# Kernel tuning notes

Measured on AMD Instinct MI355X. Metric: run time of the kernel, lower is better.

The kernel has to match this reference:

```python
import jax, jax.numpy as jnp
import numpy as np

B, S, D, F, E, K, H = 4, 1024, 512, 2048, 8, 2, 8
HEAD_DIM = D // H


def setup_inputs() -> dict:
    key = jax.random.key(0)
    ks = jax.random.split(key, 8)
    s = 0.02
    return {
        "x": jax.random.normal(ks[0], (B, S, D), jnp.float32),
        "gate_Wk": jax.random.normal(ks[1], (D, D), jnp.float32) * s,
        "gate_bk": jnp.zeros((D,), jnp.float32),
        "expert_queries": jax.random.normal(ks[2], (E, D), jnp.float32),
        "Wqkv": jax.random.normal(ks[3], (E, 3 * D, D), jnp.float32) * s,
        "bqkv": jnp.zeros((E, 3 * D), jnp.float32),
        "Wo": jax.random.normal(ks[4], (E, D, D), jnp.float32) * s,
        "bo": jnp.zeros((E, D), jnp.float32),
        "g1": jnp.ones((E, D), jnp.float32),
        "be1": jnp.zeros((E, D), jnp.float32),
        "W1": jax.random.normal(ks[5], (E, F, D), jnp.float32) * s,
        "bf1": jnp.zeros((E, F), jnp.float32),
        "W2": jax.random.normal(ks[6], (E, D, F), jnp.float32) * s,
        "bf2": jnp.zeros((E, D), jnp.float32),
        "g2": jnp.ones((E, D), jnp.float32),
        "be2": jnp.zeros((E, D), jnp.float32),
    }


def _layernorm(x, g, b):
    m = x.mean(-1, keepdims=True)
    v = ((x - m) ** 2).mean(-1, keepdims=True)
    return (x - m) * jax.lax.rsqrt(v + 1e-5) * g + b


def _expert(x, Wqkv, bqkv, Wo, bo, g1, be1, W1, bf1, W2, bf2, g2, be2):
    # x: [B,S,D]; one ExpertTransformerDecoder block (dropout=0, eval)
    b, s, d = x.shape
    qkv = x @ Wqkv.T + bqkv                      # [B,S,3D]
    q, k, v = jnp.split(qkv, 3, axis=-1)
    to_heads = lambda t: t.reshape(b, s, H, HEAD_DIM).transpose(0, 2, 1, 3)
    q, k, v = to_heads(q), to_heads(k), to_heads(v)
    scale = 1.0 / np.sqrt(HEAD_DIM).astype(np.float32)
    attn = jax.nn.softmax(jnp.einsum('bhqd,bhkd->bhqk', q * scale, k), axis=-1)
    ctx = jnp.einsum('bhqk,bhkd->bhqd', attn, v).transpose(0, 2, 1, 3).reshape(b, s, d)
    ctx = ctx @ Wo.T + bo
    x = _layernorm(x + ctx, g1, be1)
    h = jax.nn.gelu(x @ W1.T + bf1, approximate=False)
    h = jax.nn.gelu(h @ W2.T + bf2, approximate=False)
    return _layernorm(x + h, g2, be2)


def reference(x, gate_Wk, gate_bk, expert_queries, Wqkv, bqkv, Wo, bo,
              g1, be1, W1, bf1, W2, bf2, g2, be2):
    # attention gating: softmax over experts of <key_proj(x), expert_q> * d^-0.5
    keys = x @ gate_Wk.T + gate_bk                      # [B,S,D]
    scores = jnp.einsum('bsd,ed->bse', keys, expert_queries) * (D ** -0.5)
    probs = jax.nn.softmax(scores, axis=-1)             # [B,S,E]
    # top-k mask + renormalize
    _, idx = jax.lax.top_k(probs, K)                    # [B,S,K]
    mask = jax.nn.one_hot(idx, E, dtype=probs.dtype).sum(-2)
    gated = probs * mask
    gated = gated / (gated.sum(-1, keepdims=True) + 1e-9)
    # run all experts densely (as the torch code does), vmapped over E
    eo = jax.vmap(_expert, in_axes=(None,) + (0,) * 12)(
        x, Wqkv, bqkv, Wo, bo, g1, be1, W1, bf1, W2, bf2, g2, be2)  # [E,B,S,D]
    return jnp.einsum('ebsd,bse->bsd', eo, gated)
```

## Files before the change

kernel.cpp:

```cpp
#include <hip/hip_runtime.h>
#include <cstdint>
#include <cmath>

#define Bc 4
#define Sc 1024
#define Dc 512
#define Fc 2048
#define Ec 8
#define Hc 8
#define Mc 4096

typedef unsigned short u16;
typedef __attribute__((ext_vector_type(8))) short bf16x8;
typedef __attribute__((ext_vector_type(4))) float f32x4;

__device__ __forceinline__ float bf2f(u16 u) {
  unsigned v = ((unsigned)u) << 16;
  return __builtin_bit_cast(float, v);
}
__device__ __forceinline__ u16 f2bf(float f) {
  unsigned u = __builtin_bit_cast(unsigned, f);
  unsigned r = 0x7fffu + ((u >> 16) & 1u);
  return (u16)((u + r) >> 16);
}
__device__ __forceinline__ unsigned pack2bf(float a, float b) {
  return (unsigned)f2bf(a) | ((unsigned)f2bf(b) << 16);
}
__device__ __forceinline__ float gelu_f(float x) {
  const float z = 1.5957691216057308f * fmaf(0.044715f * x, x * x, x);
  const float e = __expf(z);
  return x * (1.0f - __builtin_amdgcn_rcpf(e + 1.0f));
}
__device__ __forceinline__ void async16(const void* g, void* l) {
  __builtin_amdgcn_global_load_lds(
      (const __attribute__((address_space(1))) unsigned int*)g,
      (__attribute__((address_space(3))) unsigned int*)l, 16, 0, 0);
}

__global__ __launch_bounds__(256) void cvt5_kernel(const float* __restrict__ p0, u16* __restrict__ q0,
                                                   const float* __restrict__ p1, u16* __restrict__ q1,
                                                   const float* __restrict__ p2, u16* __restrict__ q2,
                                                   const float* __restrict__ p3, u16* __restrict__ q3,
                                                   const float* __restrict__ p4, u16* __restrict__ q4) {
  int bx = blockIdx.x;
  const float* in;
  u16* outp;
  if (bx < 2048) { in = p0; outp = q0; }
  else if (bx < 8192) { in = p1; outp = q1; bx -= 2048; }
  else if (bx < 10240) { in = p2; outp = q2; bx -= 8192; }
  else if (bx < 18432) { in = p3; outp = q3; bx -= 10240; }
  else { in = p4; outp = q4; bx -= 18432; }
  const long long i = ((long long)bx * 256 + threadIdx.x) * 4;
  const float4 v = *(const float4*)(in + i);
  ushort4 o;
  o.x = f2bf(v.x); o.y = f2bf(v.y); o.z = f2bf(v.z); o.w = f2bf(v.w);
  *(ushort4*)(outp + i) = o;
}

__global__ __launch_bounds__(256) void weq_kernel(const float* __restrict__ gWk,
                                                  const float* __restrict__ eq,
                                                  float* __restrict__ weq) {
  __shared__ float red[4][64];
  const int tid = threadIdx.x, wave = tid >> 6, lane = tid & 63;
  const int d = blockIdx.x * 64 + lane;
  const int e = blockIdx.y;
  float acc = 0.f;
  for (int j = wave * 128; j < wave * 128 + 128; ++j)
    acc += gWk[(long long)j * 512 + d] * eq[e * 512 + j];
  red[wave][lane] = acc;
  __syncthreads();
  if (wave == 0)
    weq[e * 512 + d] = red[0][lane] + red[1][lane] + red[2][lane] + red[3][lane];
}
__global__ void beq_kernel(const float* __restrict__ gbk, const float* __restrict__ eq,
                           float* __restrict__ beq) {
  const int wave = threadIdx.x >> 6, lane = threadIdx.x & 63;
  for (int e = wave; e < 8; e += 4) {
    float a = 0.f;
#pragma unroll
    for (int i = 0; i < 8; ++i) a += gbk[lane + 64 * i] * eq[e * 512 + lane + 64 * i];
#pragma unroll
    for (int off = 32; off; off >>= 1) a += __shfl_xor(a, off);
    if (lane == 0) beq[e] = a;
  }
}

__global__ __launch_bounds__(256) void gate_kernel(const float* __restrict__ x,
                                                   const float* __restrict__ weq,
                                                   const float* __restrict__ beq,
                                                   float* __restrict__ gated,
                                                   int* __restrict__ cnt, int* __restrict__ tlist,
                                                   int* __restrict__ pos) {
  const int wave = threadIdx.x >> 6, lane = threadIdx.x & 63;
  const int t = blockIdx.x * 4 + wave;
  const float* xr = x + (long long)t * 512;
  float acc[8] = {};
#pragma unroll
  for (int i = 0; i < 8; ++i) {
    const float xv = xr[lane + 64 * i];
#pragma unroll
    for (int e2 = 0; e2 < 8; ++e2) acc[e2] += xv * weq[e2 * 512 + lane + 64 * i];
  }
#pragma unroll
  for (int e2 = 0; e2 < 8; ++e2)
#pragma unroll
    for (int off = 32; off; off >>= 1) acc[e2] += __shfl_xor(acc[e2], off);
  if (lane == 0) {
    const float scale = 0.044194173824159216f;
    float s[8], mx = -1e30f;
#pragma unroll
    for (int e2 = 0; e2 < 8; ++e2) { s[e2] = (acc[e2] + beq[e2]) * scale; mx = fmaxf(mx, s[e2]); }
    float p[8], sum = 0.f;
#pragma unroll
    for (int e2 = 0; e2 < 8; ++e2) { p[e2] = expf(s[e2] - mx); sum += p[e2]; }
#pragma unroll
    for (int e2 = 0; e2 < 8; ++e2) p[e2] /= sum;
    int i1 = 0;
#pragma unroll
    for (int e2 = 1; e2 < 8; ++e2) if (p[e2] > p[i1]) i1 = e2;
    int i2 = (i1 == 0) ? 1 : 0;
#pragma unroll
    for (int e2 = 0; e2 < 8; ++e2) if (e2 != i1 && e2 != i2 && p[e2] > p[i2]) i2 = e2;
    const float denom = p[i1] + p[i2] + 1e-9f;
#pragma unroll
    for (int e2 = 0; e2 < 8; ++e2)
      gated[t * 8 + e2] = (e2 == i1 || e2 == i2) ? p[e2] / denom : 0.f;
    const int b = t >> 10;
    int s1 = atomicAdd(cnt + i1 * 4 + b, 1);
    tlist[(i1 * 4 + b) * 1024 + s1] = t;
    pos[i1 * 4096 + t] = s1;
    int s2 = atomicAdd(cnt + i2 * 4 + b, 1);
    tlist[(i2 * 4 + b) * 1024 + s2] = t;
    pos[i2 * 4096 + t] = s2;
  }
}

__global__ void pad_kernel(const int* __restrict__ cnt, int* __restrict__ tlist) {
  const int seg = blockIdx.x;
  const int c = cnt[seg];
  const int ce = (c + 127) & ~127;
  const int tpad = (seg & 3) << 10;
  for (int i = c + (int)threadIdx.x; i < ce; i += 128) tlist[seg * 1024 + i] = tpad;
}

__global__ void wl_kernel(const int* __restrict__ cnt, int* __restrict__ wl) {
  const int seg = threadIdx.x;
  if (seg >= 32) return;
  int base = 0;
  for (int s = 0; s < seg; ++s) base += (cnt[s] + 127) >> 7;
  const int nt = (cnt[seg] + 127) >> 7;
  for (int t = 0; t < nt; ++t) wl[base + t] = (seg << 8) | t;
  if (seg == 31) wl[96] = base + nt;
}

template <int GELU, int QKV, int ROUTED, int BK, int GATHER>
__global__ __launch_bounds__(256) void gemm_bf16(
    const u16* __restrict__ A, const u16* __restrict__ Bw, const float* __restrict__ bias,
    u16* __restrict__ Cout, u16* __restrict__ vT, int M, int N, int K, long long Astride,
    long long Bstride, const int* __restrict__ wl, const int* __restrict__ tlist) {
  int e;
  long long bm;
  if (ROUTED) {
    const int total = wl[96];
    if ((int)blockIdx.x >= total) return;
    const int item = wl[blockIdx.x];
    const int seg = item >> 8, tile = item & 255;
    e = seg >> 2;
    bm = ((long long)(seg & 3) << 10) + tile * 128;
  } else {
    e = blockIdx.z;
    bm = (long long)blockIdx.x * 128;
  }
  __shared__ __attribute__((aligned(16))) u16 As[128 * BK];
  __shared__ __attribute__((aligned(16))) u16 Bs[128 * BK];
  const int tid = threadIdx.x;
  const int wave = tid >> 6, lane = tid & 63;
  const long long bn = (long long)blockIdx.y * 128;
  const u16* Ag = A + (long long)e * Astride + bm * K;
  const u16* Bg = Bw + ((long long)e * Bstride + bn) * K;
  constexpr int LPR = BK / 8;
  constexpr int RPI = 512 / BK;
  constexpr int IPW = BK / 16;
  const int lrow = lane / LPR, lpos = lane % LPR;
  const int lm = lane & 15, quad = lane >> 4;
  const int wm = (wave >> 1) * 64, wn = (wave & 1) * 64;
  int tok[IPW];
  if (GATHER) {
    const long long tbase = (long long)e * 4096 + bm;
#pragma unroll
    for (int i = 0; i < IPW; ++i) {
      const int gi = wave * IPW + i;
      tok[i] = tlist[tbase + gi * RPI + lrow];
    }
  }
  f32x4 acc[4][4] = {};
  for (int kk = 0; kk < K; kk += BK) {
    __syncthreads();
#pragma unroll
    for (int i = 0; i < IPW; ++i) {
      const int gi = wave * IPW + i;
      const int row = gi * RPI + lrow;
      const int sc = lpos ^ (row & 7);
      if (GATHER)
        async16(A + (long long)tok[i] * K + kk + sc * 8, &As[gi * 512]);
      else
        async16(Ag + (long long)row * K + kk + sc * 8, &As[gi * 512]);
      async16(Bg + (long long)row * K + kk + sc * 8, &Bs[gi * 512]);
    }
    __syncthreads();
#pragma unroll
    for (int ks = 0; ks < BK / 32; ++ks) {
      bf16x8 af[4], bfr[4];
#pragma unroll
      for (int mi = 0; mi < 4; ++mi) {
        const int row = wm + mi * 16 + lm;
        const int ch = (ks * 4 + quad) ^ (row & 7);
        af[mi] = *(const bf16x8*)(As + row * BK + ch * 8);
      }
#pragma unroll
      for (int nj = 0; nj < 4; ++nj) {
        const int row = wn + nj * 16 + lm;
        const int ch = (ks * 4 + quad) ^ (row & 7);
        bfr[nj] = *(const bf16x8*)(Bs + row * BK + ch * 8);
      }
#pragma unroll
      for (int mi = 0; mi < 4; ++mi)
#pragma unroll
        for (int nj = 0; nj < 4; ++nj)
          acc[mi][nj] = __builtin_amdgcn_mfma_f32_16x16x32_bf16(bfr[nj], af[mi], acc[mi][nj], 0, 0, 0);
    }
  }
  const float* bs = bias + (long long)e * Bstride;
#pragma unroll
  for (int mi = 0; mi < 4; ++mi) {
    const int m = (int)bm + wm + mi * 16 + lm;
#pragma unroll
    for (int nj = 0; nj < 4; ++nj) {
      const int n0 = (int)bn + wn + nj * 16 + quad * 4;
      const float4 bv = *(const float4*)(bs + n0);
      float v0 = acc[mi][nj][0] + bv.x;
      float v1 = acc[mi][nj][1] + bv.y;
      float v2 = acc[mi][nj][2] + bv.z;
      float v3 = acc[mi][nj][3] + bv.w;
      if (GELU) { v0 = gelu_f(v0); v1 = gelu_f(v1); v2 = gelu_f(v2); v3 = gelu_f(v3); }
      if (QKV) {
        if (n0 < 512) {
          uint2 pk; pk.x = pack2bf(v0, v1); pk.y = pack2bf(v2, v3);
          *(uint2*)(Cout + ((long long)e * Mc + m) * 512 + n0) = pk;
        } else {
          const int hh = (n0 - 512) >> 6, dd = (n0 - 512) & 63;
          const int bb = m >> 10, ss = m & 1023;
          u16* vp = vT + ((((long long)e * Bc + bb) * Hc + hh) * 64 + dd) * Sc + ss;
          vp[0] = f2bf(v0); vp[Sc] = f2bf(v1); vp[2 * Sc] = f2bf(v2); vp[3 * Sc] = f2bf(v3);
        }
      } else {
        uint2 pk; pk.x = pack2bf(v0, v1); pk.y = pack2bf(v2, v3);
        *(uint2*)(Cout + ((long long)e * M + m) * N + n0) = pk;
      }
    }
  }
}

__global__ __launch_bounds__(256, 4) void attn_tile(const u16* __restrict__ qb,
                                                    const u16* __restrict__ kb,
                                                    const u16* __restrict__ vT,
                                                    u16* __restrict__ ctx,
                                                    const int* __restrict__ wl) {
  const int idx = blockIdx.x >> 3, h = blockIdx.x & 7;
  if (idx >= wl[96]) return;
  const int item = wl[idx];
  const int seg = item >> 8, tile = item & 255;
  const int e = seg >> 2, b = seg & 3;
  __shared__ __attribute__((aligned(16))) u16 Ks[64 * 64];
  __shared__ __attribute__((aligned(16))) u16 Vs[64 * 64];
  __shared__ __attribute__((aligned(16))) u16 Pl[4][16 * 72];
  const int tid = threadIdx.x, wave = tid >> 6, lane = tid & 63;
  const int lm = lane & 15, quad = lane >> 4;
  const u16* kbase = kb + ((long long)e * Mc + b * Sc) * 512;
  const u16* vbase = vT + ((((long long)e * Bc + b) * Hc + h) * 64) * Sc;
  const int lr = lane >> 3, lc = (lane & 7) ^ lr;
  u16* P = &Pl[wave][0];
  unsigned* P32 = (unsigned*)P;
  const int pwbase = lm * 36 + quad * 2;

  const long long pidx0 = (long long)seg * 1024 + tile * 128 + wave * 16 + lm;
  bf16x8 aq[2][2];
#pragma unroll
  for (int t = 0; t < 2; ++t)
#pragma unroll
    for (int ks = 0; ks < 2; ++ks)
      aq[t][ks] = *(const bf16x8*)(qb + (pidx0 + t * 64) * 512 + h * 64 + ks * 32 + quad * 8);
  f32x4 O[2][4] = {};
  float lsum[2] = {0.f, 0.f};

  for (int n0 = 0; n0 < Sc; n0 += 64) {
    __syncthreads();
#pragma unroll
    for (int i = 0; i < 2; ++i) {
      const int rg = wave * 2 + i;
      const int row = rg * 8 + lr;
      async16(kbase + (long long)(n0 + row) * 512 + h * 64 + lc * 8, &Ks[rg * 512]);
      async16(vbase + (long long)row * Sc + n0 + lc * 8, &Vs[rg * 512]);
    }
    __syncthreads();
    bf16x8 kf[4][2];
#pragma unroll
    for (int kj = 0; kj < 4; ++kj) {
      const int row = kj * 16 + lm;
      kf[kj][0] = *(const bf16x8*)(Ks + row * 64 + ((quad) ^ (row & 7)) * 8);
      kf[kj][1] = *(const bf16x8*)(Ks + row * 64 + ((4 + quad) ^ (row & 7)) * 8);
    }
    bf16x8 ap[2][2];
#pragma unroll
    for (int t = 0; t < 2; ++t) {
      f32x4 sT[4];
#pragma unroll
      for (int kj = 0; kj < 4; ++kj) {
        f32x4 c = {};
        c = __builtin_amdgcn_mfma_f32_16x16x32_bf16(kf[kj][0], aq[t][0], c, 0, 0, 0);
        c = __builtin_amdgcn_mfma_f32_16x16x32_bf16(kf[kj][1], aq[t][1], c, 0, 0, 0);
        sT[kj] = c;
      }
#pragma unroll
      for (int kj = 0; kj < 4; ++kj) {
        const float p0 = __expf(sT[kj][0] * 0.125f);
        const float p1 = __expf(sT[kj][1] * 0.125f);
        const float p2 = __expf(sT[kj][2] * 0.125f);
        const float p3 = __expf(sT[kj][3] * 0.125f);
        lsum[t] += (p0 + p1) + (p2 + p3);
        P32[pwbase + kj * 8 + 0] = pack2bf(p0, p1);
        P32[pwbase + kj * 8 + 1] = pack2bf(p2, p3);
      }
      asm volatile("s_waitcnt lgkmcnt(0)" ::: "memory");
      ap[t][0] = *(const bf16x8*)(P + lm * 72 + quad * 8);
      ap[t][1] = *(const bf16x8*)(P + lm * 72 + 32 + quad * 8);
    }
#pragma unroll
    for (int d4 = 0; d4 < 4; ++d4) {
      const int row = d4 * 16 + lm;
      const bf16x8 v0 = *(const bf16x8*)(Vs + row * 64 + ((quad) ^ (row & 7)) * 8);
      const bf16x8 v1 = *(const bf16x8*)(Vs + row * 64 + ((4 + quad) ^ (row & 7)) * 8);
#pragma unroll
      for (int t = 0; t < 2; ++t) {
        O[t][d4] = __builtin_amdgcn_mfma_f32_16x16x32_bf16(v0, ap[t][0], O[t][d4], 0, 0, 0);
        O[t][d4] = __builtin_amdgcn_mfma_f32_16x16x32_bf16(v1, ap[t][1], O[t][d4], 0, 0, 0);
      }
    }
  }
#pragma unroll
  for (int t = 0; t < 2; ++t) {
    float ls = lsum[t];
    ls += __shfl_xor(ls, 16);
    ls += __shfl_xor(ls, 32);
    const float inv = 1.0f / ls;
#pragma unroll
    for (int d4 = 0; d4 < 4; ++d4) {
      uint2 pk;
      pk.x = pack2bf(O[t][d4][0] * inv, O[t][d4][1] * inv);
      pk.y = pack2bf(O[t][d4][2] * inv, O[t][d4][3] * inv);
      *(uint2*)(ctx + (pidx0 + t * 64) * 512 + h * 64 + d4 * 16 + quad * 4) = pk;
    }
  }
}

__global__ __launch_bounds__(256) void ln1_kernel(const float* __restrict__ x,
                                                  const u16* __restrict__ ctxp,
                                                  const float* __restrict__ g1,
                                                  const float* __restrict__ be1,
                                                  u16* __restrict__ x1,
                                                  const int* __restrict__ cnt,
                                                  const int* __restrict__ tlist) {
  const int i = blockIdx.x, b = blockIdx.y, e = blockIdx.z;
  const int seg = (e << 2) + b;
  const int ce = (cnt[seg] + 127) & ~127;
  if (i >= ce) return;
  const long long p = seg * 1024 + i;
  const int t = tlist[p];
  const int tid = threadIdx.x;
  const int wave = tid >> 6, lane = tid & 63;
  __shared__ float sred[4], qred[4];
  const float v0 = x[(long long)t * 512 + tid] + bf2f(ctxp[p * 512 + tid]);
  const float v1 = x[(long long)t * 512 + tid + 256] + bf2f(ctxp[p * 512 + tid + 256]);
  float s = v0 + v1, q = v0 * v0 + v1 * v1;
#pragma unroll
  for (int off = 32; off; off >>= 1) { s += __shfl_xor(s, off); q += __shfl_xor(q, off); }
  if (lane == 0) { sred[wave] = s; qred[wave] = q; }
  __syncthreads();
  s = sred[0] + sred[1] + sred[2] + sred[3];
  q = qred[0] + qred[1] + qred[2] + qred[3];
  const float mean = s * (1.0f / 512.0f);
  const float var = q * (1.0f / 512.0f) - mean * mean;
  const float rstd = rsqrtf(var + 1e-5f);
  x1[p * 512 + tid] = f2bf((v0 - mean) * rstd * g1[e * 512 + tid] + be1[e * 512 + tid]);
  x1[p * 512 + tid + 256] =
      f2bf((v1 - mean) * rstd * g1[e * 512 + tid + 256] + be1[e * 512 + tid + 256]);
}

__global__ __launch_bounds__(256) void ln2_kernel(const u16* __restrict__ x1,
                                                  const u16* __restrict__ h2,
                                                  const float* __restrict__ g2,
                                                  const float* __restrict__ be2,
                                                  const float* __restrict__ gated,
                                                  const int* __restrict__ pos,
                                                  float* __restrict__ out) {
  const int t = blockIdx.x, tid = threadIdx.x;
  const int b = t >> 10;
  const int wave = tid >> 6, lane = tid & 63;
  __shared__ float sred[4], qred[4];
  float o0 = 0.f, o1 = 0.f;
  for (int e = 0; e < 8; ++e) {
    const float wgt = gated[t * 8 + e];
    if (wgt != 0.f) {
      const long long p = ((e << 2) + b) * 1024 + pos[e * 4096 + t];
      const float v0 = bf2f(x1[p * 512 + tid]) + bf2f(h2[p * 512 + tid]);
      const float v1 = bf2f(x1[p * 512 + tid + 256]) + bf2f(h2[p * 512 + tid + 256]);
      float s = v0 + v1, q = v0 * v0 + v1 * v1;
#pragma unroll
      for (int off = 32; off; off >>= 1) { s += __shfl_xor(s, off); q += __shfl_xor(q, off); }
      if (lane == 0) { sred[wave] = s; qred[wave] = q; }
      __syncthreads();
      s = sred[0] + sred[1] + sred[2] + sred[3];
      q = qred[0] + qred[1] + qred[2] + qred[3];
      __syncthreads();
      const float mean = s * (1.0f / 512.0f);
      const float var = q * (1.0f / 512.0f) - mean * mean;
      const float rstd = rsqrtf(var + 1e-5f);
      o0 += wgt * ((v0 - mean) * rstd * g2[e * 512 + tid] + be2[e * 512 + tid]);
      o1 += wgt * ((v1 - mean) * rstd * g2[e * 512 + tid + 256] + be2[e * 512 + tid + 256]);
    }
  }
  out[(long long)t * 512 + tid] = o0;
  out[(long long)t * 512 + tid + 256] = o1;
}

extern "C" void kernel_launch(void* const* d_in, const int* in_sizes, int n_in, void* d_out,
                              int out_size, void* d_ws, size_t ws_size, hipStream_t stream) {
  const float* x    = (const float*)d_in[0];
  const float* gWk  = (const float*)d_in[1];
  const float* gbk  = (const float*)d_in[2];
  const float* eq   = (const float*)d_in[3];
  const float* Wqkv = (const float*)d_in[4];
  const float* bqkv = (const float*)d_in[5];
  const float* Wo   = (const float*)d_in[6];
  const float* bo   = (const float*)d_in[7];
  const float* g1   = (const float*)d_in[8];
  const float* be1  = (const float*)d_in[9];
  const float* W1   = (const float*)d_in[10];
  const float* bf1  = (const float*)d_in[11];
  const float* W2   = (const float*)d_in[12];
  const float* bf2  = (const float*)d_in[13];
  const float* g2   = (const float*)d_in[14];
  const float* be2  = (const float*)d_in[15];
  float* out = (float*)d_out;

  char* wsp = (char*)d_ws;
  size_t off = 0;
  auto take = [&](size_t bytes) -> void* {
    void* p = wsp + off;
    off += (bytes + 255) & ~(size_t)255;
    return p;
  };
  u16* xb    = (u16*)take((size_t)Mc * 512 * 2);
  u16* Wqkvb = (u16*)take((size_t)Ec * 1536 * 512 * 2);
  u16* Wob   = (u16*)take((size_t)Ec * 512 * 512 * 2);
  u16* W1b   = (u16*)take((size_t)Ec * 2048 * 512 * 2);
  u16* W2b   = (u16*)take((size_t)Ec * 512 * 2048 * 2);
  float* weq   = (float*)take(8 * 512 * 4);
  float* beqb  = (float*)take(8 * 4);
  float* gated = (float*)take((size_t)Mc * 8 * 4);
  int* cnt   = (int*)take(32 * 4);
  int* tlist = (int*)take(32 * 1024 * 4);
  int* pos   = (int*)take((size_t)Ec * Mc * 4);
  int* wl    = (int*)take(512 * 4);
  char* big = (char*)take(134217728);
  u16* qb   = (u16*)big;
  u16* kb   = (u16*)(big + 33554432);
  u16* vTb  = (u16*)(big + 67108864);
  u16* ctxp = (u16*)(big + 100663296);
  u16* hb   = (u16*)big;
  u16* ctxb = (u16*)take(33554432);
  u16* h2b  = ctxb;
  u16* x1b  = (u16*)take(33554432);
  (void)in_sizes; (void)n_in; (void)out_size; (void)ws_size;

  cvt5_kernel<<<dim3(26624), dim3(256), 0, stream>>>(x, xb, Wqkv, Wqkvb, Wo, Wob, W1, W1b, W2, W2b);
  hipMemsetAsync(cnt, 0, 32 * 4, stream);
  weq_kernel<<<dim3(8, 8), dim3(256), 0, stream>>>(gWk, eq, weq);
  beq_kernel<<<dim3(1), dim3(256), 0, stream>>>(gbk, eq, beqb);
  gate_kernel<<<dim3(1024), dim3(256), 0, stream>>>(x, weq, beqb, gated, cnt, tlist, pos);
  pad_kernel<<<dim3(32), dim3(128), 0, stream>>>(cnt, tlist);
  wl_kernel<<<dim3(1), dim3(64), 0, stream>>>(cnt, wl);
  gemm_bf16<0, 1, 0, 64, 0><<<dim3(32, 8, 8), dim3(256), 0, stream>>>(
      xb, Wqkvb + 512 * 512, bqkv + 512, kb, vTb, Mc, 1024, 512, 0LL, 1536LL, wl, nullptr);
  gemm_bf16<0, 0, 1, 128, 1><<<dim3(96, 4), dim3(256), 0, stream>>>(
      xb, Wqkvb, bqkv, qb, nullptr, Mc, 512, 512, 0LL, 1536LL, wl, tlist);
  attn_tile<<<dim3(96 * 8), dim3(256), 0, stream>>>(qb, kb, vTb, ctxb, wl);
  gemm_bf16<0, 0, 1, 128, 0><<<dim3(96, 4), dim3(256), 0, stream>>>(
      ctxb, Wob, bo, ctxp, nullptr, Mc, 512, 512, (long long)Mc * 512, 512LL, wl, nullptr);
  ln1_kernel<<<dim3(1024, 4, 8), dim3(256), 0, stream>>>(x, ctxp, g1, be1, x1b, cnt, tlist);
  gemm_bf16<1, 0, 1, 128, 0><<<dim3(96, 16), dim3(256), 0, stream>>>(
      x1b, W1b, bf1, hb, nullptr, Mc, 2048, 512, (long long)Mc * 512, 2048LL, wl, nullptr);
  gemm_bf16<1, 0, 1, 128, 0><<<dim3(96, 4), dim3(256), 0, stream>>>(
      hb, W2b, bf2, h2b, nullptr, Mc, 512, 2048, (long long)Mc * 2048, 512LL, wl, nullptr);
  ln2_kernel<<<dim3(4096), dim3(256), 0, stream>>>(x1b, h2b, g2, be2, gated, pos, out);
}
```

Before: 473.1 us.

## Add 64-row routed GEMM, split K/V projections with swapped-MFMA vectorized V^T store

Adds a 64-row-tile routed GEMM (gemm64_bf16) with its own doubled worklist, and uses it for the Q, Wo and W2 projections. The intent is to double the block count on the narrow N=512 GEMMs and cut padding waste. The fused K/V projection is split into two launches. The V launch swaps the MFMA operand order so the transposed V^T store becomes a contiguous 8-byte write instead of four scattered 2-byte writes. The costs are an extra kernel launch and lower per-block reuse of the B tile.

```diff
diff --git a/kernel.cpp b/kernel.cpp
--- a/kernel.cpp
+++ b/kernel.cpp
@@ -150,14 +150,15 @@
   for (int s = 0; s < seg; ++s) base += (cnt[s] + 127) >> 7;
   const int nt = (cnt[seg] + 127) >> 7;
   for (int t = 0; t < nt; ++t) wl[base + t] = (seg << 8) | t;
-  if (seg == 31) wl[96] = base + nt;
-}
-
-template <int GELU, int QKV, int ROUTED, int BK, int GATHER>
+  for (int t = 0; t < 2 * nt; ++t) wl[128 + 2 * base + t] = (seg << 8) | t;
+  if (seg == 31) { wl[96] = base + nt; wl[97] = 2 * (base + nt); }
+}
+
+template <int GELU, int VSWAP, int ROUTED, int BK>
 __global__ __launch_bounds__(256) void gemm_bf16(
     const u16* __restrict__ A, const u16* __restrict__ Bw, const float* __restrict__ bias,
-    u16* __restrict__ Cout, u16* __restrict__ vT, int M, int N, int K, long long Astride,
-    long long Bstride, const int* __restrict__ wl, const int* __restrict__ tlist) {
+    u16* __restrict__ Cout, int M, int N, int K, long long Astride,
+    long long Bstride, const int* __restrict__ wl) {
   int e;
   long long bm;
   if (ROUTED) {
@@ -184,15 +185,6 @@
   const int lrow = lane / LPR, lpos = lane % LPR;
   const int lm = lane & 15, quad = lane >> 4;
   const int wm = (wave >> 1) * 64, wn = (wave & 1) * 64;
-  int tok[IPW];
-  if (GATHER) {
-    const long long tbase = (long long)e * 4096 + bm;
-#pragma unroll
-    for (int i = 0; i < IPW; ++i) {
-      const int gi = wave * IPW + i;
-      tok[i] = tlist[tbase + gi * RPI + lrow];
-    }
-  }
   f32x4 acc[4][4] = {};
   for (int kk = 0; kk < K; kk += BK) {
     __syncthreads();
@@ -201,10 +193,7 @@
       const int gi = wave * IPW + i;
       const int row = gi * RPI + lrow;
       const int sc = lpos ^ (row & 7);
-      if (GATHER)
-        async16(A + (long long)tok[i] * K + kk + sc * 8, &As[gi * 512]);
-      else
-        async16(Ag + (long long)row * K + kk + sc * 8, &As[gi * 512]);
+      async16(Ag + (long long)row * K + kk + sc * 8, &As[gi * 512]);
       async16(Bg + (long long)row * K + kk + sc * 8, &Bs[gi * 512]);
     }
     __syncthreads();
@@ -226,11 +215,33 @@
 #pragma unroll
       for (int mi = 0; mi < 4; ++mi)
 #pragma unroll
-        for (int nj = 0; nj < 4; ++nj)
-          acc[mi][nj] = __builtin_amdgcn_mfma_f32_16x16x32_bf16(bfr[nj], af[mi], acc[mi][nj], 0, 0, 0);
+        for (int nj = 0; nj < 4; ++nj) {
+          if (VSWAP)
+            acc[mi][nj] = __builtin_amdgcn_mfma_f32_16x16x32_bf16(af[mi], bfr[nj], acc[mi][nj], 0, 0, 0);
+          else
+            acc[mi][nj] = __builtin_amdgcn_mfma_f32_16x16x32_bf16(bfr[nj], af[mi], acc[mi][nj], 0, 0, 0);
+        }
     }
   }
   const float* bs = bias + (long long)e * Bstride;
+  if (VSWAP) {
+#pragma unroll
+    for (int nj = 0; nj < 4; ++nj) {
+      const int n = (int)bn + wn + nj * 16 + lm;
+      const float bvs = bs[n];
+      const int hh = n >> 6, dd = n & 63;
+#pragma unroll
+      for (int mi = 0; mi < 4; ++mi) {
+        const int m0 = (int)bm + wm + mi * 16 + quad * 4;
+        const int bb = m0 >> 10, ss = m0 & 1023;
+        uint2 pk;
+        pk.x = pack2bf(acc[mi][nj][0] + bvs, acc[mi][nj][1] + bvs);
+        pk.y = pack2bf(acc[mi][nj][2] + bvs, acc[mi][nj][3] + bvs);
+        *(uint2*)(Cout + ((((long long)e * Bc + bb) * Hc + hh) * 64 + dd) * Sc + ss) = pk;
+      }
+    }
+    return;
+  }
 #pragma unroll
   for (int mi = 0; mi < 4; ++mi) {
     const int m = (int)bm + wm + mi * 16 + lm;
@@ -243,20 +254,92 @@
       float v2 = acc[mi][nj][2] + bv.z;
       float v3 = acc[mi][nj][3] + bv.w;
       if (GELU) { v0 = gelu_f(v0); v1 = gelu_f(v1); v2 = gelu_f(v2); v3 = gelu_f(v3); }
-      if (QKV) {
-        if (n0 < 512) {
-          uint2 pk; pk.x = pack2bf(v0, v1); pk.y = pack2bf(v2, v3);
-          *(uint2*)(Cout + ((long long)e * Mc + m) * 512 + n0) = pk;
-        } else {
-          const int hh = (n0 - 512) >> 6, dd = (n0 - 512) & 63;
-          const int bb = m >> 10, ss = m & 1023;
-          u16* vp = vT + ((((long long)e * Bc + bb) * Hc + hh) * 64 + dd) * Sc + ss;
-          vp[0] = f2bf(v0); vp[Sc] = f2bf(v1); vp[2 * Sc] = f2bf(v2); vp[3 * Sc] = f2bf(v3);
-        }
-      } else {
-        uint2 pk; pk.x = pack2bf(v0, v1); pk.y = pack2bf(v2, v3);
-        *(uint2*)(Cout + ((long long)e * M + m) * N + n0) = pk;
-      }
+      uint2 pk; pk.x = pack2bf(v0, v1); pk.y = pack2bf(v2, v3);
+      *(uint2*)(Cout + ((long long)e * M + m) * N + n0) = pk;
+    }
+  }
+}
+
+template <int GELU, int GATHER>
+__global__ __launch_bounds__(256) void gemm64_bf16(
+    const u16* __restrict__ A, const u16* __restrict__ Bw, const float* __restrict__ bias,
+    u16* __restrict__ Cout, int N, int K, long long Bstride,
+    const int* __restrict__ wl, const int* __restrict__ tlist) {
+  if ((int)blockIdx.x >= wl[97]) return;
+  const int item = wl[128 + blockIdx.x];
+  const int seg = item >> 8, tile = item & 255;
+  const int e = seg >> 2;
+  const long long arow0 = (long long)seg * 1024 + tile * 64;
+  __shared__ __attribute__((aligned(16))) u16 As[64 * 128];
+  __shared__ __attribute__((aligned(16))) u16 Bs[128 * 128];
+  const int tid = threadIdx.x, wave = tid >> 6, lane = tid & 63;
+  const int lrow = lane >> 4, lpos = lane & 15;
+  const int lm = lane & 15, quad = lane >> 4;
+  const long long bn = (long long)blockIdx.y * 128;
+  const u16* Bg = Bw + ((long long)e * Bstride + bn) * K;
+  int tok[4];
+  if (GATHER) {
+#pragma unroll
+    for (int i = 0; i < 4; ++i) tok[i] = tlist[arow0 + (wave * 4 + i) * 4 + lrow];
+  }
+  f32x4 acc[4][2] = {};
+  for (int kk = 0; kk < K; kk += 128) {
+    __syncthreads();
+#pragma unroll
+    for (int i = 0; i < 4; ++i) {
+      const int gi = wave * 4 + i;
+      const int row = gi * 4 + lrow;
+      const int sc = lpos ^ (row & 7);
+      if (GATHER)
+        async16(A + (long long)tok[i] * K + kk + sc * 8, &As[gi * 512]);
+      else
+        async16(A + (arow0 + row) * K + kk + sc * 8, &As[gi * 512]);
+    }
+#pragma unroll
+    for (int i = 0; i < 8; ++i) {
+      const int gi = wave * 8 + i;
+      const int row = gi * 4 + lrow;
+      const int sc = lpos ^ (row & 7);
+      async16(Bg + (long long)row * K + kk + sc * 8, &Bs[gi * 512]);
+    }
+    __syncthreads();
+#pragma unroll
+    for (int ks = 0; ks < 4; ++ks) {
+      bf16x8 af[4], bfr[2];
+#pragma unroll
+      for (int mi = 0; mi < 4; ++mi) {
+        const int row = mi * 16 + lm;
+        const int ch = (ks * 4 + quad) ^ (row & 7);
+        af[mi] = *(const bf16x8*)(As + row * 128 + ch * 8);
+      }
+#pragma unroll
+      for (int nj = 0; nj < 2; ++nj) {
+        const int row = wave * 32 + nj * 16 + lm;
+        const int ch = (ks * 4 + quad) ^ (row & 7);
+        bfr[nj] = *(const bf16x8*)(Bs + row * 128 + ch * 8);
+      }
+#pragma unroll
+      for (int mi = 0; mi < 4; ++mi)
+#pragma unroll
+        for (int nj = 0; nj < 2; ++nj)
+          acc[mi][nj] = __builtin_amdgcn_mfma_f32_16x16x32_bf16(bfr[nj], af[mi], acc[mi][nj], 0, 0, 0);
+    }
+  }
+  const float* bs = bias + (long long)e * Bstride;
+#pragma unroll
+  for (int mi = 0; mi < 4; ++mi) {
+    const long long p = arow0 + mi * 16 + lm;
+#pragma unroll
+    for (int nj = 0; nj < 2; ++nj) {
+      const int n0 = (int)bn + wave * 32 + nj * 16 + quad * 4;
+      const float4 bv = *(const float4*)(bs + n0);
+      float v0 = acc[mi][nj][0] + bv.x;
+      float v1 = acc[mi][nj][1] + bv.y;
+      float v2 = acc[mi][nj][2] + bv.z;
+      float v3 = acc[mi][nj][3] + bv.w;
+      if (GELU) { v0 = gelu_f(v0); v1 = gelu_f(v1); v2 = gelu_f(v2); v3 = gelu_f(v3); }
+      uint2 pk; pk.x = pack2bf(v0, v1); pk.y = pack2bf(v2, v3);
+      *(uint2*)(Cout + p * N + n0) = pk;
     }
   }
 }
@@ -490,17 +573,19 @@
   gate_kernel<<<dim3(1024), dim3(256), 0, stream>>>(x, weq, beqb, gated, cnt, tlist, pos);
   pad_kernel<<<dim3(32), dim3(128), 0, stream>>>(cnt, tlist);
   wl_kernel<<<dim3(1), dim3(64), 0, stream>>>(cnt, wl);
-  gemm_bf16<0, 1, 0, 64, 0><<<dim3(32, 8, 8), dim3(256), 0, stream>>>(
-      xb, Wqkvb + 512 * 512, bqkv + 512, kb, vTb, Mc, 1024, 512, 0LL, 1536LL, wl, nullptr);
-  gemm_bf16<0, 0, 1, 128, 1><<<dim3(96, 4), dim3(256), 0, stream>>>(
-      xb, Wqkvb, bqkv, qb, nullptr, Mc, 512, 512, 0LL, 1536LL, wl, tlist);
+  gemm_bf16<0, 0, 0, 64><<<dim3(32, 4, 8), dim3(256), 0, stream>>>(
+      xb, Wqkvb + 512 * 512, bqkv + 512, kb, Mc, 512, 512, 0LL, 1536LL, wl);
+  gemm_bf16<0, 1, 0, 64><<<dim3(32, 4, 8), dim3(256), 0, stream>>>(
+      xb, Wqkvb + 1024 * 512, bqkv + 1024, vTb, Mc, 512, 512, 0LL, 1536LL, wl);
+  gemm64_bf16<0, 1><<<dim3(192, 4), dim3(256), 0, stream>>>(
+      xb, Wqkvb, bqkv, qb, 512, 512, 1536LL, wl, tlist);
   attn_tile<<<dim3(96 * 8), dim3(256), 0, stream>>>(qb, kb, vTb, ctxb, wl);
-  gemm_bf16<0, 0, 1, 128, 0><<<dim3(96, 4), dim3(256), 0, stream>>>(
-      ctxb, Wob, bo, ctxp, nullptr, Mc, 512, 512, (long long)Mc * 512, 512LL, wl, nullptr);
+  gemm64_bf16<0, 0><<<dim3(192, 4), dim3(256), 0, stream>>>(
+      ctxb, Wob, bo, ctxp, 512, 512, 512LL, wl, nullptr);
   ln1_kernel<<<dim3(1024, 4, 8), dim3(256), 0, stream>>>(x, ctxp, g1, be1, x1b, cnt, tlist);
-  gemm_bf16<1, 0, 1, 128, 0><<<dim3(96, 16), dim3(256), 0, stream>>>(
-      x1b, W1b, bf1, hb, nullptr, Mc, 2048, 512, (long long)Mc * 512, 2048LL, wl, nullptr);
-  gemm_bf16<1, 0, 1, 128, 0><<<dim3(96, 4), dim3(256), 0, stream>>>(
-      hb, W2b, bf2, h2b, nullptr, Mc, 512, 2048, (long long)Mc * 2048, 512LL, wl, nullptr);
+  gemm_bf16<1, 0, 1, 128><<<dim3(96, 16), dim3(256), 0, stream>>>(
+      x1b, W1b, bf1, hb, Mc, 2048, 512, (long long)Mc * 512, 2048LL, wl);
+  gemm64_bf16<1, 0><<<dim3(192, 4), dim3(256), 0, stream>>>(
+      hb, W2b, bf2, h2b, 512, 2048, 512LL, wl, nullptr);
   ln2_kernel<<<dim3(4096), dim3(256), 0, stream>>>(x1b, h2b, g2, be2, gated, pos, out);
 }
```

Measured after the change: 474.7 us. About the same (+0.4%).
